# Performance work log

Measured on AMD Instinct MI355X. Metric: run time of the kernel, lower is better.

Reference implementation:

```python
import jax, jax.numpy as jnp
import numpy as np

# Problem sizes (see shape_source): N points, D embedding dim, B subbatches (events), M labels per event.
N, D, B, M = 2_097_152, 16, 8, 32
DELTA_V, DELTA_D = 0.5, 1.5  # module defaults
EPS = 1e-8


def setup_inputs() -> dict:
    key = jax.random.key(0)
    outputs = jax.random.normal(key, (N, D), dtype=jnp.float32)
    idx = jnp.arange(N)
    # contiguous subbatches, every label present in every subbatch (matches torch.unique structure)
    subbatch_indices = (idx // (N // B)).astype(jnp.int32)
    labels = (idx % M).astype(jnp.int32)
    return {"outputs": outputs, "labels": labels, "subbatch_indices": subbatch_indices}


def reference(outputs, labels, subbatch_indices):
    # normalize=True: L2-normalize each embedding row (note: torch adds eps to the norm, not norm+eps clamp)
    x = outputs / (jnp.linalg.norm(outputs, axis=1) + EPS)[:, None]

    # flat segment id per (subbatch, label) group; every group is populated by construction
    seg = (subbatch_indices * M + labels).astype(jnp.int32)  # [N] in [0, B*M)

    ones = jnp.ones((x.shape[0],), x.dtype)
    counts = jax.ops.segment_sum(ones, seg, num_segments=B * M)        # [B*M] == Nm per group
    mus = jax.ops.segment_sum(x, seg, num_segments=B * M) / counts[:, None]  # [B*M, D] centroids

    # L_pull: per-point hinge on L1 distance to its centroid, weights are all-ones (use_weights=False)
    dist = jnp.sum(jnp.abs(mus[seg] - x), axis=1)                       # [N] L1 distance
    L_pull = jnp.sum(jax.nn.relu(dist - DELTA_V) ** 2 / (M * counts[seg]))

    # L_push: all-pairs centroid hinge within each subbatch, diagonal zeroed
    mus_b = mus.reshape(B, M, D)
    pd = jnp.sum(jnp.abs(mus_b[:, :, None, :] - mus_b[:, None, :, :]), axis=-1)  # [B, M, M]
    hinge = jax.nn.relu(2.0 * DELTA_D - pd) ** 2
    hinge = jnp.where(jnp.eye(M, dtype=bool)[None], 0.0, hinge)
    L_push = jnp.sum(hinge) / (M * (M - 1))

    return (L_pull + L_push) / B
```

## Files before the change

kernel.cpp:

```cpp
#include <hip/hip_runtime.h>
#include <math.h>


#define DD 16
#define MM 32
#define BBATCH 8
#define SEGS 256
#define DELTA_V 0.5f
#define DELTA_D 1.5f
#define NEPS 1e-8f

#define NBLK 1024
#define NTHR 256
#define CHUNK 2048

#define WS_ZERO_FLOATS 4352

__device__ __forceinline__ void lds_fadd(float* p, float v) {
    __hip_atomic_fetch_add(p, v, __ATOMIC_RELAXED, __HIP_MEMORY_SCOPE_WORKGROUP);
}

__device__ __forceinline__ float block_reduce_sum(float v) {
    #pragma unroll
    for (int o = 32; o > 0; o >>= 1) v += __shfl_down(v, o, 64);
    __shared__ float red[4];
    int wid  = threadIdx.x >> 6;
    int lane = threadIdx.x & 63;
    if (lane == 0) red[wid] = v;
    __syncthreads();
    v = (threadIdx.x < (NTHR >> 6)) ? red[threadIdx.x] : 0.0f;
    if (wid == 0) {
        #pragma unroll
        for (int o = 32; o > 0; o >>= 1) v += __shfl_down(v, o, 64);
    }
    return v;
}

__global__ void __launch_bounds__(NTHR, 4)
k_segsum(const float4* __restrict__ o4,
         const int* __restrict__ labels,
         const int* __restrict__ sub,
         float* __restrict__ seg_sum,
         float* __restrict__ seg_cnt,
         int n) {
    __shared__ float lsT[(DD + 1) * SEGS];
    for (int i = threadIdx.x; i < (DD + 1) * SEGS; i += NTHR) lsT[i] = 0.0f;
    __syncthreads();

    float4 a0 = {0,0,0,0}, a1 = {0,0,0,0}, a2 = {0,0,0,0}, a3 = {0,0,0,0};
    float cnt = 0.0f;
    int cur = -1;

    const int base = blockIdx.x * CHUNK + threadIdx.x;
    #pragma unroll
    for (int it = 0; it < CHUNK / NTHR; ++it) {
        int p = base + it * NTHR;
        if (p >= n) break;
        float4 a = o4[4 * p + 0];
        float4 b = o4[4 * p + 1];
        float4 c = o4[4 * p + 2];
        float4 e = o4[4 * p + 3];
        int seg = sub[p] * MM + labels[p];
        float ss = a.x*a.x + a.y*a.y + a.z*a.z + a.w*a.w
                 + b.x*b.x + b.y*b.y + b.z*b.z + b.w*b.w
                 + c.x*c.x + c.y*c.y + c.z*c.z + c.w*c.w
                 + e.x*e.x + e.y*e.y + e.z*e.z + e.w*e.w;
        float rn = 1.0f / (sqrtf(ss) + NEPS);
        if (seg != cur) {
            if (cur >= 0) {
                lds_fadd(&lsT[ 0*SEGS + cur], a0.x); lds_fadd(&lsT[ 1*SEGS + cur], a0.y);
                lds_fadd(&lsT[ 2*SEGS + cur], a0.z); lds_fadd(&lsT[ 3*SEGS + cur], a0.w);
                lds_fadd(&lsT[ 4*SEGS + cur], a1.x); lds_fadd(&lsT[ 5*SEGS + cur], a1.y);
                lds_fadd(&lsT[ 6*SEGS + cur], a1.z); lds_fadd(&lsT[ 7*SEGS + cur], a1.w);
                lds_fadd(&lsT[ 8*SEGS + cur], a2.x); lds_fadd(&lsT[ 9*SEGS + cur], a2.y);
                lds_fadd(&lsT[10*SEGS + cur], a2.z); lds_fadd(&lsT[11*SEGS + cur], a2.w);
                lds_fadd(&lsT[12*SEGS + cur], a3.x); lds_fadd(&lsT[13*SEGS + cur], a3.y);
                lds_fadd(&lsT[14*SEGS + cur], a3.z); lds_fadd(&lsT[15*SEGS + cur], a3.w);
                lds_fadd(&lsT[16*SEGS + cur], cnt);
            }
            a0 = a1 = a2 = a3 = (float4){0,0,0,0};
            cnt = 0.0f;
            cur = seg;
        }
        a0.x += a.x * rn; a0.y += a.y * rn; a0.z += a.z * rn; a0.w += a.w * rn;
        a1.x += b.x * rn; a1.y += b.y * rn; a1.z += b.z * rn; a1.w += b.w * rn;
        a2.x += c.x * rn; a2.y += c.y * rn; a2.z += c.z * rn; a2.w += c.w * rn;
        a3.x += e.x * rn; a3.y += e.y * rn; a3.z += e.z * rn; a3.w += e.w * rn;
        cnt += 1.0f;
    }
    if (cur >= 0) {
        lds_fadd(&lsT[ 0*SEGS + cur], a0.x); lds_fadd(&lsT[ 1*SEGS + cur], a0.y);
        lds_fadd(&lsT[ 2*SEGS + cur], a0.z); lds_fadd(&lsT[ 3*SEGS + cur], a0.w);
        lds_fadd(&lsT[ 4*SEGS + cur], a1.x); lds_fadd(&lsT[ 5*SEGS + cur], a1.y);
        lds_fadd(&lsT[ 6*SEGS + cur], a1.z); lds_fadd(&lsT[ 7*SEGS + cur], a1.w);
        lds_fadd(&lsT[ 8*SEGS + cur], a2.x); lds_fadd(&lsT[ 9*SEGS + cur], a2.y);
        lds_fadd(&lsT[10*SEGS + cur], a2.z); lds_fadd(&lsT[11*SEGS + cur], a2.w);
        lds_fadd(&lsT[12*SEGS + cur], a3.x); lds_fadd(&lsT[13*SEGS + cur], a3.y);
        lds_fadd(&lsT[14*SEGS + cur], a3.z); lds_fadd(&lsT[15*SEGS + cur], a3.w);
        lds_fadd(&lsT[16*SEGS + cur], cnt);
    }
    __syncthreads();
    for (int s = threadIdx.x; s < SEGS; s += NTHR) {
        float c = lsT[DD * SEGS + s];
        if (c != 0.0f) {
            #pragma unroll
            for (int d = 0; d < DD; ++d)
                unsafeAtomicAdd(&seg_sum[s * DD + d], lsT[d * SEGS + s]);
            unsafeAtomicAdd(&seg_cnt[s], c);
        }
    }
}

__global__ void k_finalize_push(float* __restrict__ ws) {
    const float* seg_sum = ws;
    const float* seg_cnt = ws + 4096;
    float* mus  = ws + 4352;
    float* invw = ws + 8448;
    float* push = ws + 8704;

    __shared__ float muT[DD * SEGS];
    int t = threadIdx.x;
    float cnt = seg_cnt[t];
    float ic  = (cnt > 0.0f) ? 1.0f / cnt : 0.0f;
    #pragma unroll
    for (int d = 0; d < DD; ++d) {
        float m = seg_sum[t * DD + d] * ic;
        mus[t * DD + d]   = m;
        muT[d * SEGS + t] = m;
    }
    invw[t] = (cnt > 0.0f) ? 1.0f / ((float)MM * cnt) : 0.0f;
    __syncthreads();

    int b = t >> 5, m1 = t & 31;
    float acc = 0.0f;
    for (int m2 = 0; m2 < MM; ++m2) {
        float pd = 0.0f;
        #pragma unroll
        for (int d = 0; d < DD; ++d)
            pd += fabsf(muT[d * SEGS + b * MM + m1] - muT[d * SEGS + b * MM + m2]);
        float h = 2.0f * DELTA_D - pd;
        if (m2 != m1 && h > 0.0f) acc += h * h;
    }
    float tot = block_reduce_sum(acc);
    if (t == 0) push[0] = tot / (float)(MM * (MM - 1));
}

__global__ void __launch_bounds__(NTHR, 4)
k_pull(const float4* __restrict__ o4,
       const int* __restrict__ labels,
       const int* __restrict__ sub,
       const float* __restrict__ mus,
       const float* __restrict__ invw,
       float* __restrict__ pull_part,
       int n) {
    __shared__ float muL[DD * SEGS];
    __shared__ float siw[SEGS];
    for (int i = threadIdx.x; i < DD * SEGS; i += NTHR) muL[i] = mus[i];
    for (int i = threadIdx.x; i < SEGS; i += NTHR) siw[i] = invw[i];
    __syncthreads();

    float4 m0, m1, m2, m3;
    float iw = 0.0f;
    int cur = -1;
    float acc = 0.0f;

    const int base = blockIdx.x * CHUNK + threadIdx.x;
    #pragma unroll
    for (int it = 0; it < CHUNK / NTHR; ++it) {
        int p = base + it * NTHR;
        if (p >= n) break;
        float4 a = o4[4 * p + 0];
        float4 b = o4[4 * p + 1];
        float4 c = o4[4 * p + 2];
        float4 e = o4[4 * p + 3];
        int seg = sub[p] * MM + labels[p];
        if (seg != cur) {
            cur = seg;
            m0 = *(const float4*)&muL[seg * DD +  0];
            m1 = *(const float4*)&muL[seg * DD +  4];
            m2 = *(const float4*)&muL[seg * DD +  8];
            m3 = *(const float4*)&muL[seg * DD + 12];
            iw = siw[seg];
        }
        float ss = a.x*a.x + a.y*a.y + a.z*a.z + a.w*a.w
                 + b.x*b.x + b.y*b.y + b.z*b.z + b.w*b.w
                 + c.x*c.x + c.y*c.y + c.z*c.z + c.w*c.w
                 + e.x*e.x + e.y*e.y + e.z*e.z + e.w*e.w;
        float rn = 1.0f / (sqrtf(ss) + NEPS);
        float dist;
        dist  = fabsf(m0.x - a.x * rn) + fabsf(m0.y - a.y * rn)
              + fabsf(m0.z - a.z * rn) + fabsf(m0.w - a.w * rn);
        dist += fabsf(m1.x - b.x * rn) + fabsf(m1.y - b.y * rn)
              + fabsf(m1.z - b.z * rn) + fabsf(m1.w - b.w * rn);
        dist += fabsf(m2.x - c.x * rn) + fabsf(m2.y - c.y * rn)
              + fabsf(m2.z - c.z * rn) + fabsf(m2.w - c.w * rn);
        dist += fabsf(m3.x - e.x * rn) + fabsf(m3.y - e.y * rn)
              + fabsf(m3.z - e.z * rn) + fabsf(m3.w - e.w * rn);
        float h = dist - DELTA_V;
        if (h > 0.0f) acc = fmaf(h * h, iw, acc);
    }
    float tot = block_reduce_sum(acc);
    if (threadIdx.x == 0) pull_part[blockIdx.x] = tot;
}

__global__ void k_final(const float* __restrict__ ws, float* __restrict__ out) {
    const float* push      = ws + 8704;
    const float* pull_part = ws + 8720;
    int t = threadIdx.x;
    float v = 0.0f;
    #pragma unroll
    for (int k = 0; k < NBLK / NTHR; ++k) v += pull_part[t + k * NTHR];
    float tot = block_reduce_sum(v);
    if (t == 0) out[0] = (tot + push[0]) * (1.0f / (float)BBATCH);
}

extern "C" void kernel_launch(void* const* d_in, const int* in_sizes, int n_in,
                              void* d_out, int out_size, void* d_ws, size_t ws_size,
                              hipStream_t stream) {
    const float* outputs = (const float*)d_in[0];
    const int* labels    = (const int*)d_in[1];
    const int* sub       = (const int*)d_in[2];
    int n = in_sizes[0] / DD;

    float* ws        = (float*)d_ws;
    float* seg_sum   = ws;
    float* seg_cnt   = ws + 4096;
    float* mus       = ws + 4352;
    float* invw      = ws + 8448;
    float* pull_part = ws + 8720;

    hipMemsetAsync(d_ws, 0, WS_ZERO_FLOATS * sizeof(float), stream);

    k_segsum<<<NBLK, NTHR, 0, stream>>>((const float4*)outputs, labels, sub,
                                        seg_sum, seg_cnt, n);
    k_finalize_push<<<1, NTHR, 0, stream>>>(ws);
    k_pull<<<NBLK, NTHR, 0, stream>>>((const float4*)outputs, labels, sub,
                                      mus, invw, pull_part, n);
    k_final<<<1, NTHR, 0, stream>>>(ws, (float*)d_out);
}
```

Baseline: 320.1 us.

## Split each point across four lanes for coalesced float4 loads with shuffle reductions

```diff
diff --git a/kernel.cpp b/kernel.cpp
--- a/kernel.cpp
+++ b/kernel.cpp
@@ -10,9 +10,11 @@
 #define DELTA_D 1.5f
 #define NEPS 1e-8f
 
-#define NBLK 1024
+#define NBLK 2048
 #define NTHR 256
-#define CHUNK 2048
+#define SLOTS_PER_BLK 4096
+#define UF 8
+#define ROUNDS (SLOTS_PER_BLK / (NTHR * UF))
 
 #define WS_ZERO_FLOATS 4352
 
@@ -34,6 +36,15 @@
         for (int o = 32; o > 0; o >>= 1) v += __shfl_down(v, o, 64);
     }
     return v;
+}
+
+__device__ __forceinline__ void flush_slice(float* lsT, int seg, int j,
+                                            float4 a, float cnt, bool cnt_lane) {
+    lds_fadd(&lsT[(4*j + 0) * SEGS + seg], a.x);
+    lds_fadd(&lsT[(4*j + 1) * SEGS + seg], a.y);
+    lds_fadd(&lsT[(4*j + 2) * SEGS + seg], a.z);
+    lds_fadd(&lsT[(4*j + 3) * SEGS + seg], a.w);
+    if (cnt_lane) lds_fadd(&lsT[DD * SEGS + seg], cnt);
 }
 
 __global__ void __launch_bounds__(NTHR, 4)
@@ -47,59 +58,77 @@
     for (int i = threadIdx.x; i < (DD + 1) * SEGS; i += NTHR) lsT[i] = 0.0f;
     __syncthreads();
 
-    float4 a0 = {0,0,0,0}, a1 = {0,0,0,0}, a2 = {0,0,0,0}, a3 = {0,0,0,0};
+    const int t = threadIdx.x;
+    const int j = t & 3;
+    const bool cnt_lane = (j == 0);
+    const long nslot = 4L * (long)n;
+    const long base  = (long)blockIdx.x * SLOTS_PER_BLK + t;
+
+    float4 acc = {0, 0, 0, 0};
     float cnt = 0.0f;
     int cur = -1;
 
-    const int base = blockIdx.x * CHUNK + threadIdx.x;
-    #pragma unroll
-    for (int it = 0; it < CHUNK / NTHR; ++it) {
-        int p = base + it * NTHR;
-        if (p >= n) break;
-        float4 a = o4[4 * p + 0];
-        float4 b = o4[4 * p + 1];
-        float4 c = o4[4 * p + 2];
-        float4 e = o4[4 * p + 3];
-        int seg = sub[p] * MM + labels[p];
-        float ss = a.x*a.x + a.y*a.y + a.z*a.z + a.w*a.w
-                 + b.x*b.x + b.y*b.y + b.z*b.z + b.w*b.w
-                 + c.x*c.x + c.y*c.y + c.z*c.z + c.w*c.w
-                 + e.x*e.x + e.y*e.y + e.z*e.z + e.w*e.w;
-        float rn = 1.0f / (sqrtf(ss) + NEPS);
-        if (seg != cur) {
-            if (cur >= 0) {
-                lds_fadd(&lsT[ 0*SEGS + cur], a0.x); lds_fadd(&lsT[ 1*SEGS + cur], a0.y);
-                lds_fadd(&lsT[ 2*SEGS + cur], a0.z); lds_fadd(&lsT[ 3*SEGS + cur], a0.w);
-                lds_fadd(&lsT[ 4*SEGS + cur], a1.x); lds_fadd(&lsT[ 5*SEGS + cur], a1.y);
-                lds_fadd(&lsT[ 6*SEGS + cur], a1.z); lds_fadd(&lsT[ 7*SEGS + cur], a1.w);
-                lds_fadd(&lsT[ 8*SEGS + cur], a2.x); lds_fadd(&lsT[ 9*SEGS + cur], a2.y);
-                lds_fadd(&lsT[10*SEGS + cur], a2.z); lds_fadd(&lsT[11*SEGS + cur], a2.w);
-                lds_fadd(&lsT[12*SEGS + cur], a3.x); lds_fadd(&lsT[13*SEGS + cur], a3.y);
-                lds_fadd(&lsT[14*SEGS + cur], a3.z); lds_fadd(&lsT[15*SEGS + cur], a3.w);
-                lds_fadd(&lsT[16*SEGS + cur], cnt);
-            }
-            a0 = a1 = a2 = a3 = (float4){0,0,0,0};
-            cnt = 0.0f;
-            cur = seg;
-        }
-        a0.x += a.x * rn; a0.y += a.y * rn; a0.z += a.z * rn; a0.w += a.w * rn;
-        a1.x += b.x * rn; a1.y += b.y * rn; a1.z += b.z * rn; a1.w += b.w * rn;
-        a2.x += c.x * rn; a2.y += c.y * rn; a2.z += c.z * rn; a2.w += c.w * rn;
-        a3.x += e.x * rn; a3.y += e.y * rn; a3.z += e.z * rn; a3.w += e.w * rn;
-        cnt += 1.0f;
-    }
-    if (cur >= 0) {
-        lds_fadd(&lsT[ 0*SEGS + cur], a0.x); lds_fadd(&lsT[ 1*SEGS + cur], a0.y);
-        lds_fadd(&lsT[ 2*SEGS + cur], a0.z); lds_fadd(&lsT[ 3*SEGS + cur], a0.w);
-        lds_fadd(&lsT[ 4*SEGS + cur], a1.x); lds_fadd(&lsT[ 5*SEGS + cur], a1.y);
-        lds_fadd(&lsT[ 6*SEGS + cur], a1.z); lds_fadd(&lsT[ 7*SEGS + cur], a1.w);
-        lds_fadd(&lsT[ 8*SEGS + cur], a2.x); lds_fadd(&lsT[ 9*SEGS + cur], a2.y);
-        lds_fadd(&lsT[10*SEGS + cur], a2.z); lds_fadd(&lsT[11*SEGS + cur], a2.w);
-        lds_fadd(&lsT[12*SEGS + cur], a3.x); lds_fadd(&lsT[13*SEGS + cur], a3.y);
-        lds_fadd(&lsT[14*SEGS + cur], a3.z); lds_fadd(&lsT[15*SEGS + cur], a3.w);
-        lds_fadd(&lsT[16*SEGS + cur], cnt);
-    }
-    __syncthreads();
+    const bool full = ((long)(blockIdx.x + 1) * SLOTS_PER_BLK) <= nslot;
+    if (full) {
+        #pragma unroll
+        for (int r = 0; r < ROUNDS; ++r) {
+            float4 v[UF]; int lb[UF], sb[UF];
+            #pragma unroll
+            for (int u = 0; u < UF; ++u) {
+                int q = (int)base + (r * UF + u) * NTHR;
+                v[u] = o4[q];
+                int p = q >> 2;
+                lb[u] = labels[p];
+                sb[u] = sub[p];
+            }
+            #pragma unroll
+            for (int u = 0; u < UF; ++u) {
+                int seg = sb[u] * MM + lb[u];
+                float ssp = v[u].x*v[u].x + v[u].y*v[u].y
+                          + v[u].z*v[u].z + v[u].w*v[u].w;
+                ssp += __shfl_xor(ssp, 1, 64);
+                ssp += __shfl_xor(ssp, 2, 64);
+                float rn = 1.0f / (sqrtf(ssp) + NEPS);
+                if (seg != cur) {
+                    if (cur >= 0) flush_slice(lsT, cur, j, acc, cnt, cnt_lane);
+                    acc = (float4){0, 0, 0, 0};
+                    cnt = 0.0f;
+                    cur = seg;
+                }
+                acc.x = fmaf(v[u].x, rn, acc.x);
+                acc.y = fmaf(v[u].y, rn, acc.y);
+                acc.z = fmaf(v[u].z, rn, acc.z);
+                acc.w = fmaf(v[u].w, rn, acc.w);
+                cnt += 1.0f;
+            }
+        }
+    } else {
+        for (int k = 0; k < SLOTS_PER_BLK / NTHR; ++k) {
+            long q = base + (long)k * NTHR;
+            if (q >= nslot) break;
+            float4 v = o4[q];
+            int p = (int)(q >> 2);
+            int seg = sub[p] * MM + labels[p];
+            float ssp = v.x*v.x + v.y*v.y + v.z*v.z + v.w*v.w;
+            ssp += __shfl_xor(ssp, 1, 64);
+            ssp += __shfl_xor(ssp, 2, 64);
+            float rn = 1.0f / (sqrtf(ssp) + NEPS);
+            if (seg != cur) {
+                if (cur >= 0) flush_slice(lsT, cur, j, acc, cnt, cnt_lane);
+                acc = (float4){0, 0, 0, 0};
+                cnt = 0.0f;
+                cur = seg;
+            }
+            acc.x = fmaf(v.x, rn, acc.x);
+            acc.y = fmaf(v.y, rn, acc.y);
+            acc.z = fmaf(v.z, rn, acc.z);
+            acc.w = fmaf(v.w, rn, acc.w);
+            cnt += 1.0f;
+        }
+    }
+    if (cur >= 0) flush_slice(lsT, cur, j, acc, cnt, cnt_lane);
+    __syncthreads();
+
     for (int s = threadIdx.x; s < SEGS; s += NTHR) {
         float c = lsT[DD * SEGS + s];
         if (c != 0.0f) {
@@ -159,45 +188,74 @@
     for (int i = threadIdx.x; i < SEGS; i += NTHR) siw[i] = invw[i];
     __syncthreads();
 
-    float4 m0, m1, m2, m3;
-    float iw = 0.0f;
+    const int t = threadIdx.x;
+    const int j = t & 3;
+    const bool cnt_lane = (j == 0);
+    const long nslot = 4L * (long)n;
+    const long base  = (long)blockIdx.x * SLOTS_PER_BLK + t;
+
+    float4 m = {0, 0, 0, 0};
+    float iwl = 0.0f;
     int cur = -1;
     float acc = 0.0f;
 
-    const int base = blockIdx.x * CHUNK + threadIdx.x;
-    #pragma unroll
-    for (int it = 0; it < CHUNK / NTHR; ++it) {
-        int p = base + it * NTHR;
-        if (p >= n) break;
-        float4 a = o4[4 * p + 0];
-        float4 b = o4[4 * p + 1];
-        float4 c = o4[4 * p + 2];
-        float4 e = o4[4 * p + 3];
-        int seg = sub[p] * MM + labels[p];
-        if (seg != cur) {
-            cur = seg;
-            m0 = *(const float4*)&muL[seg * DD +  0];
-            m1 = *(const float4*)&muL[seg * DD +  4];
-            m2 = *(const float4*)&muL[seg * DD +  8];
-            m3 = *(const float4*)&muL[seg * DD + 12];
-            iw = siw[seg];
-        }
-        float ss = a.x*a.x + a.y*a.y + a.z*a.z + a.w*a.w
-                 + b.x*b.x + b.y*b.y + b.z*b.z + b.w*b.w
-                 + c.x*c.x + c.y*c.y + c.z*c.z + c.w*c.w
-                 + e.x*e.x + e.y*e.y + e.z*e.z + e.w*e.w;
-        float rn = 1.0f / (sqrtf(ss) + NEPS);
-        float dist;
-        dist  = fabsf(m0.x - a.x * rn) + fabsf(m0.y - a.y * rn)
-              + fabsf(m0.z - a.z * rn) + fabsf(m0.w - a.w * rn);
-        dist += fabsf(m1.x - b.x * rn) + fabsf(m1.y - b.y * rn)
-              + fabsf(m1.z - b.z * rn) + fabsf(m1.w - b.w * rn);
-        dist += fabsf(m2.x - c.x * rn) + fabsf(m2.y - c.y * rn)
-              + fabsf(m2.z - c.z * rn) + fabsf(m2.w - c.w * rn);
-        dist += fabsf(m3.x - e.x * rn) + fabsf(m3.y - e.y * rn)
-              + fabsf(m3.z - e.z * rn) + fabsf(m3.w - e.w * rn);
-        float h = dist - DELTA_V;
-        if (h > 0.0f) acc = fmaf(h * h, iw, acc);
+    const bool full = ((long)(blockIdx.x + 1) * SLOTS_PER_BLK) <= nslot;
+    if (full) {
+        #pragma unroll
+        for (int r = 0; r < ROUNDS; ++r) {
+            float4 v[UF]; int lb[UF], sb[UF];
+            #pragma unroll
+            for (int u = 0; u < UF; ++u) {
+                int q = (int)base + (r * UF + u) * NTHR;
+                v[u] = o4[q];
+                int p = q >> 2;
+                lb[u] = labels[p];
+                sb[u] = sub[p];
+            }
+            #pragma unroll
+            for (int u = 0; u < UF; ++u) {
+                int seg = sb[u] * MM + lb[u];
+                if (seg != cur) {
+                    cur = seg;
+                    m = *(const float4*)&muL[seg * DD + 4 * j];
+                    iwl = cnt_lane ? siw[seg] : 0.0f;
+                }
+                float ssp = v[u].x*v[u].x + v[u].y*v[u].y
+                          + v[u].z*v[u].z + v[u].w*v[u].w;
+                ssp += __shfl_xor(ssp, 1, 64);
+                ssp += __shfl_xor(ssp, 2, 64);
+                float rn = 1.0f / (sqrtf(ssp) + NEPS);
+                float d = fabsf(m.x - v[u].x * rn) + fabsf(m.y - v[u].y * rn)
+                        + fabsf(m.z - v[u].z * rn) + fabsf(m.w - v[u].w * rn);
+                d += __shfl_xor(d, 1, 64);
+                d += __shfl_xor(d, 2, 64);
+                float h = d - DELTA_V;
+                if (h > 0.0f) acc = fmaf(h * h, iwl, acc);
+            }
+        }
+    } else {
+        for (int k = 0; k < SLOTS_PER_BLK / NTHR; ++k) {
+            long q = base + (long)k * NTHR;
+            if (q >= nslot) break;
+            float4 v = o4[q];
+            int p = (int)(q >> 2);
+            int seg = sub[p] * MM + labels[p];
+            if (seg != cur) {
+                cur = seg;
+                m = *(const float4*)&muL[seg * DD + 4 * j];
+                iwl = cnt_lane ? siw[seg] : 0.0f;
+            }
+            float ssp = v.x*v.x + v.y*v.y + v.z*v.z + v.w*v.w;
+            ssp += __shfl_xor(ssp, 1, 64);
+            ssp += __shfl_xor(ssp, 2, 64);
+            float rn = 1.0f / (sqrtf(ssp) + NEPS);
+            float d = fabsf(m.x - v.x * rn) + fabsf(m.y - v.y * rn)
+                    + fabsf(m.z - v.z * rn) + fabsf(m.w - v.w * rn);
+            d += __shfl_xor(d, 1, 64);
+            d += __shfl_xor(d, 2, 64);
+            float h = d - DELTA_V;
+            if (h > 0.0f) acc = fmaf(h * h, iwl, acc);
+        }
     }
     float tot = block_reduce_sum(acc);
     if (threadIdx.x == 0) pull_part[blockIdx.x] = tot;
```

New measurement: 415.3 us. 1.3x slower.

## Spread segment atomics over partial copies and use more, smaller blocks

Applied to the files above, without the earlier changes.

```diff
diff --git a/kernel.cpp b/kernel.cpp
--- a/kernel.cpp
+++ b/kernel.cpp
@@ -10,11 +10,18 @@
 #define DELTA_D 1.5f
 #define NEPS 1e-8f
 
-#define NBLK 1024
 #define NTHR 256
-#define CHUNK 2048
-
-#define WS_ZERO_FLOATS 4352
+#define PPT 2
+#define CHUNK (NTHR * PPT)
+#define KP 32
+#define MAXBLK 8192
+
+#define OFF_PP    0
+#define OFF_MUS   (KP * 4352)
+#define OFF_INVW  (OFF_MUS + 4096)
+#define OFF_PUSH  (OFF_INVW + 256)
+#define OFF_PULL  (OFF_PUSH + 16)
+#define WS_ZERO_FLOATS (KP * 4352)
 
 __device__ __forceinline__ void lds_fadd(float* p, float v) {
     __hip_atomic_fetch_add(p, v, __ATOMIC_RELAXED, __HIP_MEMORY_SCOPE_WORKGROUP);
@@ -36,95 +43,103 @@
     return v;
 }
 
-__global__ void __launch_bounds__(NTHR, 4)
+__device__ __forceinline__ void flush_point(float* lsT, int seg,
+                                            float4 a0, float4 a1,
+                                            float4 a2, float4 a3, float cnt) {
+    lds_fadd(&lsT[ 0*SEGS + seg], a0.x); lds_fadd(&lsT[ 1*SEGS + seg], a0.y);
+    lds_fadd(&lsT[ 2*SEGS + seg], a0.z); lds_fadd(&lsT[ 3*SEGS + seg], a0.w);
+    lds_fadd(&lsT[ 4*SEGS + seg], a1.x); lds_fadd(&lsT[ 5*SEGS + seg], a1.y);
+    lds_fadd(&lsT[ 6*SEGS + seg], a1.z); lds_fadd(&lsT[ 7*SEGS + seg], a1.w);
+    lds_fadd(&lsT[ 8*SEGS + seg], a2.x); lds_fadd(&lsT[ 9*SEGS + seg], a2.y);
+    lds_fadd(&lsT[10*SEGS + seg], a2.z); lds_fadd(&lsT[11*SEGS + seg], a2.w);
+    lds_fadd(&lsT[12*SEGS + seg], a3.x); lds_fadd(&lsT[13*SEGS + seg], a3.y);
+    lds_fadd(&lsT[14*SEGS + seg], a3.z); lds_fadd(&lsT[15*SEGS + seg], a3.w);
+    lds_fadd(&lsT[16*SEGS + seg], cnt);
+}
+
+__global__ void __launch_bounds__(NTHR, 8)
 k_segsum(const float4* __restrict__ o4,
          const int* __restrict__ labels,
          const int* __restrict__ sub,
-         float* __restrict__ seg_sum,
-         float* __restrict__ seg_cnt,
+         float* __restrict__ pp,
          int n) {
     __shared__ float lsT[(DD + 1) * SEGS];
     for (int i = threadIdx.x; i < (DD + 1) * SEGS; i += NTHR) lsT[i] = 0.0f;
     __syncthreads();
 
-    float4 a0 = {0,0,0,0}, a1 = {0,0,0,0}, a2 = {0,0,0,0}, a3 = {0,0,0,0};
+    float4 c0 = {0,0,0,0}, c1 = {0,0,0,0}, c2 = {0,0,0,0}, c3 = {0,0,0,0};
     float cnt = 0.0f;
     int cur = -1;
 
-    const int base = blockIdx.x * CHUNK + threadIdx.x;
-    #pragma unroll
-    for (int it = 0; it < CHUNK / NTHR; ++it) {
-        int p = base + it * NTHR;
-        if (p >= n) break;
-        float4 a = o4[4 * p + 0];
-        float4 b = o4[4 * p + 1];
-        float4 c = o4[4 * p + 2];
-        float4 e = o4[4 * p + 3];
-        int seg = sub[p] * MM + labels[p];
-        float ss = a.x*a.x + a.y*a.y + a.z*a.z + a.w*a.w
-                 + b.x*b.x + b.y*b.y + b.z*b.z + b.w*b.w
-                 + c.x*c.x + c.y*c.y + c.z*c.z + c.w*c.w
-                 + e.x*e.x + e.y*e.y + e.z*e.z + e.w*e.w;
-        float rn = 1.0f / (sqrtf(ss) + NEPS);
-        if (seg != cur) {
-            if (cur >= 0) {
-                lds_fadd(&lsT[ 0*SEGS + cur], a0.x); lds_fadd(&lsT[ 1*SEGS + cur], a0.y);
-                lds_fadd(&lsT[ 2*SEGS + cur], a0.z); lds_fadd(&lsT[ 3*SEGS + cur], a0.w);
-                lds_fadd(&lsT[ 4*SEGS + cur], a1.x); lds_fadd(&lsT[ 5*SEGS + cur], a1.y);
-                lds_fadd(&lsT[ 6*SEGS + cur], a1.z); lds_fadd(&lsT[ 7*SEGS + cur], a1.w);
-                lds_fadd(&lsT[ 8*SEGS + cur], a2.x); lds_fadd(&lsT[ 9*SEGS + cur], a2.y);
-                lds_fadd(&lsT[10*SEGS + cur], a2.z); lds_fadd(&lsT[11*SEGS + cur], a2.w);
-                lds_fadd(&lsT[12*SEGS + cur], a3.x); lds_fadd(&lsT[13*SEGS + cur], a3.y);
-                lds_fadd(&lsT[14*SEGS + cur], a3.z); lds_fadd(&lsT[15*SEGS + cur], a3.w);
-                lds_fadd(&lsT[16*SEGS + cur], cnt);
+    for (long cb = blockIdx.x; cb * CHUNK < (long)n; cb += gridDim.x) {
+        const int pbase = (int)(cb * CHUNK) + threadIdx.x;
+        #pragma unroll
+        for (int u = 0; u < PPT; ++u) {
+            int p = pbase + u * NTHR;
+            if (p >= n) break;
+            int lb = labels[p];
+            int sv = sub[p];
+            float4 a = o4[4*p+0], b = o4[4*p+1], c = o4[4*p+2], e = o4[4*p+3];
+            int seg = sv * MM + lb;
+            float ss = a.x*a.x + a.y*a.y + a.z*a.z + a.w*a.w
+                     + b.x*b.x + b.y*b.y + b.z*b.z + b.w*b.w
+                     + c.x*c.x + c.y*c.y + c.z*c.z + c.w*c.w
+                     + e.x*e.x + e.y*e.y + e.z*e.z + e.w*e.w;
+            float rn = 1.0f / (sqrtf(ss) + NEPS);
+            if (seg != cur) {
+                if (cur >= 0) flush_point(lsT, cur, c0, c1, c2, c3, cnt);
+                c0 = c1 = c2 = c3 = (float4){0,0,0,0};
+                cnt = 0.0f;
+                cur = seg;
             }
-            a0 = a1 = a2 = a3 = (float4){0,0,0,0};
-            cnt = 0.0f;
-            cur = seg;
+            c0.x = fmaf(a.x, rn, c0.x); c0.y = fmaf(a.y, rn, c0.y);
+            c0.z = fmaf(a.z, rn, c0.z); c0.w = fmaf(a.w, rn, c0.w);
+            c1.x = fmaf(b.x, rn, c1.x); c1.y = fmaf(b.y, rn, c1.y);
+            c1.z = fmaf(b.z, rn, c1.z); c1.w = fmaf(b.w, rn, c1.w);
+            c2.x = fmaf(c.x, rn, c2.x); c2.y = fmaf(c.y, rn, c2.y);
+            c2.z = fmaf(c.z, rn, c2.z); c2.w = fmaf(c.w, rn, c2.w);
+            c3.x = fmaf(e.x, rn, c3.x); c3.y = fmaf(e.y, rn, c3.y);
+            c3.z = fmaf(e.z, rn, c3.z); c3.w = fmaf(e.w, rn, c3.w);
+            cnt += 1.0f;
         }
-        a0.x += a.x * rn; a0.y += a.y * rn; a0.z += a.z * rn; a0.w += a.w * rn;
-        a1.x += b.x * rn; a1.y += b.y * rn; a1.z += b.z * rn; a1.w += b.w * rn;
-        a2.x += c.x * rn; a2.y += c.y * rn; a2.z += c.z * rn; a2.w += c.w * rn;
-        a3.x += e.x * rn; a3.y += e.y * rn; a3.z += e.z * rn; a3.w += e.w * rn;
-        cnt += 1.0f;
-    }
-    if (cur >= 0) {
-        lds_fadd(&lsT[ 0*SEGS + cur], a0.x); lds_fadd(&lsT[ 1*SEGS + cur], a0.y);
-        lds_fadd(&lsT[ 2*SEGS + cur], a0.z); lds_fadd(&lsT[ 3*SEGS + cur], a0.w);
-        lds_fadd(&lsT[ 4*SEGS + cur], a1.x); lds_fadd(&lsT[ 5*SEGS + cur], a1.y);
-        lds_fadd(&lsT[ 6*SEGS + cur], a1.z); lds_fadd(&lsT[ 7*SEGS + cur], a1.w);
-        lds_fadd(&lsT[ 8*SEGS + cur], a2.x); lds_fadd(&lsT[ 9*SEGS + cur], a2.y);
-        lds_fadd(&lsT[10*SEGS + cur], a2.z); lds_fadd(&lsT[11*SEGS + cur], a2.w);
-        lds_fadd(&lsT[12*SEGS + cur], a3.x); lds_fadd(&lsT[13*SEGS + cur], a3.y);
-        lds_fadd(&lsT[14*SEGS + cur], a3.z); lds_fadd(&lsT[15*SEGS + cur], a3.w);
-        lds_fadd(&lsT[16*SEGS + cur], cnt);
-    }
-    __syncthreads();
+    }
+    if (cur >= 0) flush_point(lsT, cur, c0, c1, c2, c3, cnt);
+    __syncthreads();
+
+    float* dst = pp + (size_t)(blockIdx.x & (KP - 1)) * (SEGS * 17);
     for (int s = threadIdx.x; s < SEGS; s += NTHR) {
         float c = lsT[DD * SEGS + s];
         if (c != 0.0f) {
             #pragma unroll
             for (int d = 0; d < DD; ++d)
-                unsafeAtomicAdd(&seg_sum[s * DD + d], lsT[d * SEGS + s]);
-            unsafeAtomicAdd(&seg_cnt[s], c);
+                unsafeAtomicAdd(&dst[s * 17 + d], lsT[d * SEGS + s]);
+            unsafeAtomicAdd(&dst[s * 17 + 16], c);
         }
     }
 }
 
 __global__ void k_finalize_push(float* __restrict__ ws) {
-    const float* seg_sum = ws;
-    const float* seg_cnt = ws + 4096;
-    float* mus  = ws + 4352;
-    float* invw = ws + 8448;
-    float* push = ws + 8704;
+    const float* pp = ws + OFF_PP;
+    float* mus  = ws + OFF_MUS;
+    float* invw = ws + OFF_INVW;
+    float* push = ws + OFF_PUSH;
 
     __shared__ float muT[DD * SEGS];
     int t = threadIdx.x;
-    float cnt = seg_cnt[t];
+
+    float s17[DD + 1];
+    #pragma unroll
+    for (int d = 0; d <= DD; ++d) s17[d] = 0.0f;
+    for (int k = 0; k < KP; ++k) {
+        const float* src = pp + (size_t)k * (SEGS * 17) + t * 17;
+        #pragma unroll
+        for (int d = 0; d <= DD; ++d) s17[d] += src[d];
+    }
+    float cnt = s17[DD];
     float ic  = (cnt > 0.0f) ? 1.0f / cnt : 0.0f;
     #pragma unroll
     for (int d = 0; d < DD; ++d) {
-        float m = seg_sum[t * DD + d] * ic;
+        float m = s17[d] * ic;
         mus[t * DD + d]   = m;
         muT[d * SEGS + t] = m;
     }
@@ -145,7 +160,7 @@
     if (t == 0) push[0] = tot / (float)(MM * (MM - 1));
 }
 
-__global__ void __launch_bounds__(NTHR, 4)
+__global__ void __launch_bounds__(NTHR, 8)
 k_pull(const float4* __restrict__ o4,
        const int* __restrict__ labels,
        const int* __restrict__ sub,
@@ -164,52 +179,53 @@
     int cur = -1;
     float acc = 0.0f;
 
-    const int base = blockIdx.x * CHUNK + threadIdx.x;
-    #pragma unroll
-    for (int it = 0; it < CHUNK / NTHR; ++it) {
-        int p = base + it * NTHR;
-        if (p >= n) break;
-        float4 a = o4[4 * p + 0];
-        float4 b = o4[4 * p + 1];
-        float4 c = o4[4 * p + 2];
-        float4 e = o4[4 * p + 3];
-        int seg = sub[p] * MM + labels[p];
-        if (seg != cur) {
-            cur = seg;
-            m0 = *(const float4*)&muL[seg * DD +  0];
-            m1 = *(const float4*)&muL[seg * DD +  4];
-            m2 = *(const float4*)&muL[seg * DD +  8];
-            m3 = *(const float4*)&muL[seg * DD + 12];
-            iw = siw[seg];
+    for (long cb = blockIdx.x; cb * CHUNK < (long)n; cb += gridDim.x) {
+        const int pbase = (int)(cb * CHUNK) + threadIdx.x;
+        #pragma unroll
+        for (int u = 0; u < PPT; ++u) {
+            int p = pbase + u * NTHR;
+            if (p >= n) break;
+            int lb = labels[p];
+            int sv = sub[p];
+            float4 a = o4[4*p+0], b = o4[4*p+1], c = o4[4*p+2], e = o4[4*p+3];
+            int seg = sv * MM + lb;
+            if (seg != cur) {
+                cur = seg;
+                m0 = *(const float4*)&muL[seg * DD +  0];
+                m1 = *(const float4*)&muL[seg * DD +  4];
+                m2 = *(const float4*)&muL[seg * DD +  8];
+                m3 = *(const float4*)&muL[seg * DD + 12];
+                iw = siw[seg];
+            }
+            float ss = a.x*a.x + a.y*a.y + a.z*a.z + a.w*a.w
+                     + b.x*b.x + b.y*b.y + b.z*b.z + b.w*b.w
+                     + c.x*c.x + c.y*c.y + c.z*c.z + c.w*c.w
+                     + e.x*e.x + e.y*e.y + e.z*e.z + e.w*e.w;
+            float rn = 1.0f / (sqrtf(ss) + NEPS);
+            float dist;
+            dist  = fabsf(m0.x - a.x * rn) + fabsf(m0.y - a.y * rn)
+                  + fabsf(m0.z - a.z * rn) + fabsf(m0.w - a.w * rn);
+            dist += fabsf(m1.x - b.x * rn) + fabsf(m1.y - b.y * rn)
+                  + fabsf(m1.z - b.z * rn) + fabsf(m1.w - b.w * rn);
+            dist += fabsf(m2.x - c.x * rn) + fabsf(m2.y - c.y * rn)
+                  + fabsf(m2.z - c.z * rn) + fabsf(m2.w - c.w * rn);
+            dist += fabsf(m3.x - e.x * rn) + fabsf(m3.y - e.y * rn)
+                  + fabsf(m3.z - e.z * rn) + fabsf(m3.w - e.w * rn);
+            float h = dist - DELTA_V;
+            if (h > 0.0f) acc = fmaf(h * h, iw, acc);
         }
-        float ss = a.x*a.x + a.y*a.y + a.z*a.z + a.w*a.w
-                 + b.x*b.x + b.y*b.y + b.z*b.z + b.w*b.w
-                 + c.x*c.x + c.y*c.y + c.z*c.z + c.w*c.w
-                 + e.x*e.x + e.y*e.y + e.z*e.z + e.w*e.w;
-        float rn = 1.0f / (sqrtf(ss) + NEPS);
-        float dist;
-        dist  = fabsf(m0.x - a.x * rn) + fabsf(m0.y - a.y * rn)
-              + fabsf(m0.z - a.z * rn) + fabsf(m0.w - a.w * rn);
-        dist += fabsf(m1.x - b.x * rn) + fabsf(m1.y - b.y * rn)
-              + fabsf(m1.z - b.z * rn) + fabsf(m1.w - b.w * rn);
-        dist += fabsf(m2.x - c.x * rn) + fabsf(m2.y - c.y * rn)
-              + fabsf(m2.z - c.z * rn) + fabsf(m2.w - c.w * rn);
-        dist += fabsf(m3.x - e.x * rn) + fabsf(m3.y - e.y * rn)
-              + fabsf(m3.z - e.z * rn) + fabsf(m3.w - e.w * rn);
-        float h = dist - DELTA_V;
-        if (h > 0.0f) acc = fmaf(h * h, iw, acc);
     }
     float tot = block_reduce_sum(acc);
     if (threadIdx.x == 0) pull_part[blockIdx.x] = tot;
 }
 
-__global__ void k_final(const float* __restrict__ ws, float* __restrict__ out) {
-    const float* push      = ws + 8704;
-    const float* pull_part = ws + 8720;
+__global__ void k_final(const float* __restrict__ ws, float* __restrict__ out,
+                        int nblk) {
+    const float* push      = ws + OFF_PUSH;
+    const float* pull_part = ws + OFF_PULL;
     int t = threadIdx.x;
     float v = 0.0f;
-    #pragma unroll
-    for (int k = 0; k < NBLK / NTHR; ++k) v += pull_part[t + k * NTHR];
+    for (int k = t; k < nblk; k += NTHR) v += pull_part[k];
     float tot = block_reduce_sum(v);
     if (t == 0) out[0] = (tot + push[0]) * (1.0f / (float)BBATCH);
 }
@@ -223,18 +239,20 @@
     int n = in_sizes[0] / DD;
 
     float* ws        = (float*)d_ws;
-    float* seg_sum   = ws;
-    float* seg_cnt   = ws + 4096;
-    float* mus       = ws + 4352;
-    float* invw      = ws + 8448;
-    float* pull_part = ws + 8720;
-
-    hipMemsetAsync(d_ws, 0, WS_ZERO_FLOATS * sizeof(float), stream);
-
-    k_segsum<<<NBLK, NTHR, 0, stream>>>((const float4*)outputs, labels, sub,
-                                        seg_sum, seg_cnt, n);
+    float* pp        = ws + OFF_PP;
+    float* mus       = ws + OFF_MUS;
+    float* invw      = ws + OFF_INVW;
+    float* pull_part = ws + OFF_PULL;
+
+    long nblk_l = ((long)n + CHUNK - 1) / CHUNK;
+    int nblk = (nblk_l > MAXBLK) ? MAXBLK : (int)nblk_l;
+
+    hipMemsetAsync(d_ws, 0, (size_t)WS_ZERO_FLOATS * sizeof(float), stream);
+
+    k_segsum<<<nblk, NTHR, 0, stream>>>((const float4*)outputs, labels, sub,
+                                        pp, n);
     k_finalize_push<<<1, NTHR, 0, stream>>>(ws);
-    k_pull<<<NBLK, NTHR, 0, stream>>>((const float4*)outputs, labels, sub,
+    k_pull<<<nblk, NTHR, 0, stream>>>((const float4*)outputs, labels, sub,
                                       mus, invw, pull_part, n);
-    k_final<<<1, NTHR, 0, stream>>>(ws, (float*)d_out);
-}
+    k_final<<<1, NTHR, 0, stream>>>(ws, (float*)d_out, nblk);
+}
```

New measurement: 391.5 us. +22.3%, slower.
